# Kernel tuning notes

Hardware: AMD Instinct MI355X
Metric: run time of the kernel (lower is better)

Reference implementation:

```python
import jax, jax.numpy as jnp
import numpy as np

B, IN_DIM, N, L = 8, 2, 512, 64
D_MODEL = 32
D_FF = 32          # must equal D_MODEL: output_bn is BatchNorm2d(d_model) applied to skip
DEPTH = 3          # blocks=3 * layers=1; dilation resets to 1 each block -> all dilations = 1
KS = 2             # temporal kernel size
EPS = 1e-5         # BatchNorm eps


def setup_inputs() -> dict:
    key = jax.random.key(0)
    ks = jax.random.split(key, 16)
    s = 0.1  # weight scale for numeric sanity
    x = jax.random.normal(ks[0], (B, IN_DIM, N, L), jnp.float32)
    a = jax.random.uniform(ks[1], (N, N), jnp.float32)
    adj = a / a.sum(axis=1, keepdims=True)  # row-stochastic diffusion matrix
    return {
        "x": x,
        "adj": adj,
        "Wstart": jax.random.normal(ks[2], (D_MODEL, IN_DIM), jnp.float32) * s,
        "bstart": jnp.zeros((D_MODEL,), jnp.float32),
        "Wf": jax.random.normal(ks[3], (DEPTH, D_MODEL, D_MODEL, KS), jnp.float32) * s,
        "bf": jnp.zeros((DEPTH, D_MODEL), jnp.float32),
        "Wg": jax.random.normal(ks[4], (DEPTH, D_MODEL, D_MODEL, KS), jnp.float32) * s,
        "bg": jnp.zeros((DEPTH, D_MODEL), jnp.float32),
        "Wskip": jax.random.normal(ks[5], (DEPTH, D_FF, D_MODEL), jnp.float32) * s,
        "bskip": jnp.zeros((DEPTH, D_FF), jnp.float32),
        "Wgc": jax.random.normal(ks[6], (DEPTH, D_MODEL, 3 * D_MODEL), jnp.float32) * s,
        "bgc": jnp.zeros((DEPTH, D_MODEL), jnp.float32),
        "gcbn_g": jnp.ones((DEPTH, D_MODEL), jnp.float32),
        "gcbn_b": jnp.zeros((DEPTH, D_MODEL), jnp.float32),
        "bn_g": jnp.ones((DEPTH, D_MODEL), jnp.float32),
        "bn_b": jnp.zeros((DEPTH, D_MODEL), jnp.float32),
        "obn_g": jnp.ones((D_MODEL,), jnp.float32),
        "obn_b": jnp.zeros((D_MODEL,), jnp.float32),
    }


def _c1x1(x, W, b):
    # Conv2d with (1,1) kernel == channel mixing. x: [b,c,n,l], W: [o,c]
    return jnp.einsum('bcnl,oc->bonl', x, W) + b[None, :, None, None]


def _dconv(x, W, b, d):
    # Conv2d kernel (1,2), dilation d along time (valid). W: [o,c,2]
    Lx = x.shape[-1]
    y = (jnp.einsum('bcnl,oc->bonl', x[..., :Lx - d], W[..., 0])
         + jnp.einsum('bcnl,oc->bonl', x[..., d:], W[..., 1]))
    return y + b[None, :, None, None]


def _bn(x, g, bta):
    # eval-mode BatchNorm2d: running_mean=0, running_var=1
    inv = g / jnp.sqrt(1.0 + EPS)
    return x * inv[None, :, None, None] + bta[None, :, None, None]


def reference(x, adj, Wstart, bstart, Wf, bf, Wg, bg, Wskip, bskip,
              Wgc, bgc, gcbn_g, gcbn_b, bn_g, bn_b, obn_g, obn_b):
    rf = 1 + DEPTH * (KS - 1)  # receptive field with dilation 1 per layer
    h = _c1x1(x, Wstart, bstart)
    if h.shape[-1] < rf:
        h = jnp.pad(h, ((0, 0), (0, 0), (0, 0), (rf - h.shape[-1], 0)))
    skip = None
    for i in range(DEPTH):
        residual = h
        filt = jnp.tanh(_dconv(h, Wf[i], bf[i], 1))
        gate = jax.nn.sigmoid(_dconv(h, Wg[i], bg[i], 1))
        h = filt * gate
        s = _c1x1(h, Wskip[i], bskip[i])
        skip = s if skip is None else s + skip[..., -s.shape[-1]:]
        if i == DEPTH - 1:
            break
        # order-2 graph diffusion: h, A h, A^2 h -> concat -> 1x1 conv -> BN (dropout: eval noop)
        x1 = jnp.einsum('bcnl,nm->bcml', h, adj)
        x2 = jnp.einsum('bcnl,nm->bcml', x1, adj)
        cat = jnp.concatenate([h, x1, x2], axis=1)
        g = _bn(_c1x1(cat, Wgc[i], bgc[i]), gcbn_g[i], gcbn_b[i])
        h = g + residual[..., -g.shape[-1]:]
        h = _bn(h, bn_g[i], bn_b[i])
    out = _bn(skip, obn_g, obn_b)
    return jnp.swapaxes(out, 1, 3)  # [B, L', N, C]
```

## Files before the change

### kernel.cpp

```cpp
#include <hip/hip_runtime.h>
#include <hip/hip_bf16.h>

#define B_     8
#define CIN_   2
#define N_     512
#define C_     32
#define L_     64
#define LOUT_  61
#define BUF_   ((size_t)(8*32*512*64))

typedef __hip_bfloat16 bf16;
typedef unsigned short ushort_t;
typedef __attribute__((ext_vector_type(8))) unsigned short us8;
typedef __attribute__((ext_vector_type(8))) short bf16x8;
typedef __attribute__((ext_vector_type(4))) float f32x4;

static __device__ __forceinline__ float bits2f(ushort_t u) {
    return __uint_as_float(((unsigned)u) << 16);
}
static __device__ __forceinline__ ushort_t f2bits(float v) {
    unsigned u = __float_as_uint(v);
    return (ushort_t)((u + 0x7fffu + ((u >> 16) & 1u)) >> 16);
}

__global__ void k_start(const float* __restrict__ x,
                        const float* __restrict__ Wst,
                        const float* __restrict__ bst,
                        ushort_t* __restrict__ h) {
    int idx = blockIdx.x * 256 + threadIdx.x;
    int l0 = (idx & 7) * 8;
    int n  = (idx >> 3) & 511;
    int o  = (idx >> 12) & 31;
    int b  = idx >> 17;
    float w0 = Wst[o * 2], w1 = Wst[o * 2 + 1], bb = bst[o];
    int xbase = (b * CIN_ * N_ + n) * L_ + l0;
    float va[8], vb[8];
    *(float4*)&va[0] = *(const float4*)(x + xbase);
    *(float4*)&va[4] = *(const float4*)(x + xbase + 4);
    *(float4*)&vb[0] = *(const float4*)(x + xbase + N_ * L_);
    *(float4*)&vb[4] = *(const float4*)(x + xbase + N_ * L_ + 4);
    us8 r;
    #pragma unroll
    for (int k = 0; k < 8; ++k) r[k] = f2bits(bb + va[k] * w0 + vb[k] * w1);
    *(us8*)(h + (size_t)idx * 8) = r;
}

__global__ void k_transA(const float* __restrict__ adj, ushort_t* __restrict__ adjT) {
    __shared__ float buf[64][65];
    int ti = blockIdx.x & 7;
    int tj = blockIdx.x >> 3;
    int t = threadIdx.x;
    for (int r = 0; r < 16; ++r) {
        int e = t + 256 * r;
        int rl = e >> 6, cl = e & 63;
        buf[rl][cl] = adj[(size_t)(ti * 64 + rl) * 512 + tj * 64 + cl];
    }
    __syncthreads();
    for (int r = 0; r < 16; ++r) {
        int e = t + 256 * r;
        int ml = e >> 6, nl = e & 63;
        adjT[(size_t)(tj * 64 + ml) * 512 + ti * 64 + nl] = f2bits(buf[nl][ml]);
    }
}

__global__ __launch_bounds__(256, 2) void k_sq(const ushort_t* __restrict__ adjT,
                                               ushort_t* __restrict__ adj2T) {
    __shared__ __align__(16) ushort_t lds2[8192];
    ushort_t* As = lds2;
    ushort_t* Bs = lds2 + 4096;
    int mt = blockIdx.x & 7, nc = blockIdx.x >> 3;
    int t = threadIdx.x, lane = t & 63, w = t >> 6;
    int la = lane & 15, q = lane >> 4;
    f32x4 acc[4];
    #pragma unroll
    for (int mi = 0; mi < 4; ++mi) acc[mi] = (f32x4)0.f;
    for (int p0 = 0; p0 < 512; p0 += 64) {
        __syncthreads();
        #pragma unroll
        for (int r = 0; r < 2; ++r) {
            int e = t + 256 * r, ml = e >> 3, oct = e & 7;
            int sw = ((oct + (ml >> 3)) & 7) << 3;
            *(us8*)(As + ml * 64 + sw) =
                *(const us8*)(adjT + (size_t)(mt * 64 + ml) * 512 + p0 + oct * 8);
            *(us8*)(Bs + ml * 64 + sw) =
                *(const us8*)(adjT + (size_t)(p0 + ml) * 512 + nc * 64 + oct * 8);
        }
        __syncthreads();
        #pragma unroll
        for (int ks = 0; ks < 2; ++ks) {
            bf16x8 a[4];
            #pragma unroll
            for (int mi = 0; mi < 4; ++mi) {
                int m = mi * 16 + la;
                int bl = (ks * 4 + q + (m >> 3)) & 7;
                a[mi] = *(const bf16x8*)(As + m * 64 + bl * 8);
            }
            bf16x8 bv;
            {
                int n = w * 16 + la;
                int rot = ((n >> 3) + ks * 4 + q) & 7;
                int col = rot * 8 + (n & 7);
                const ushort_t* p = Bs + (ks * 32 + q * 8) * 64 + col;
                #pragma unroll
                for (int j = 0; j < 8; ++j) bv[j] = (short)p[j * 64];
            }
            #pragma unroll
            for (int mi = 0; mi < 4; ++mi)
                acc[mi] = __builtin_amdgcn_mfma_f32_16x16x32_bf16(a[mi], bv, acc[mi], 0, 0, 0);
        }
    }
    __syncthreads();
    ushort_t* Ys = lds2;
    #pragma unroll
    for (int mi = 0; mi < 4; ++mi)
        #pragma unroll
        for (int r = 0; r < 4; ++r)
            Ys[(mi * 16 + q * 4 + r) * 72 + w * 16 + la] = f2bits(acc[mi][r]);
    __syncthreads();
    #pragma unroll
    for (int r = 0; r < 2; ++r) {
        int e = t + 256 * r, ml = e >> 3, oct = e & 7;
        us8 v = *(const us8*)(Ys + ml * 72 + oct * 8);
        *(us8*)(adj2T + (size_t)(mt * 64 + ml) * 512 + nc * 64 + oct * 8) = v;
    }
}

__global__ __launch_bounds__(256, 2) void k_gs_mfma(
        const ushort_t* __restrict__ h,
        const float* __restrict__ Wf, const float* __restrict__ bfp,
        const float* __restrict__ Wg, const float* __restrict__ bgp,
        const float* __restrict__ Wsk, const float* __restrict__ bsk,
        ushort_t* __restrict__ G, float* __restrict__ out,
        int off, int mode, int storeG,
        const float* __restrict__ og, const float* __restrict__ obb) {
    __shared__ __align__(16) ushort_t Hs[128 * 72];
    __shared__ __align__(16) ushort_t Asf[32 * 72];
    __shared__ __align__(16) ushort_t Asg[32 * 72];
    __shared__ __align__(16) ushort_t As2[32 * 40];
    __shared__ float bfv[32], bgv[32], bsv[32];
    int t = threadIdx.x;
    int b = blockIdx.x >> 7, n0 = (blockIdx.x & 127) * 4;
    int lane = t & 63, w = t >> 6;
    int la = lane & 15, q = lane >> 4;

    {
        int o = t >> 3, k8 = (t & 7) * 8;
        us8 vf, vg;
        #pragma unroll
        for (int i = 0; i < 8; ++i) {
            int k = k8 + i, c = k & 31, tap = k >> 5;
            vf[i] = f2bits(Wf[o * 64 + c * 2 + tap]);
            vg[i] = f2bits(Wg[o * 64 + c * 2 + tap]);
        }
        *(us8*)(Asf + o * 72 + k8) = vf;
        *(us8*)(Asg + o * 72 + k8) = vg;
        if (k8 < 32) {
            us8 vs;
            #pragma unroll
            for (int i = 0; i < 8; ++i) vs[i] = f2bits(Wsk[o * 32 + k8 + i]);
            *(us8*)(As2 + o * 40 + k8) = vs;
        }
        if (t < 32) { bfv[t] = bfp[t]; bgv[t] = bgp[t]; bsv[t] = bsk[t]; }
    }
    const ushort_t* hb = h + (size_t)(b * 32) * 512 * 64;
    #pragma unroll
    for (int r = 0; r < 4; ++r) {
        int e = t + 256 * r;
        int row = e >> 3, oct = e & 7;
        us8 v = *(const us8*)(hb + ((size_t)(row >> 2) * 512 + n0 + (row & 3)) * 64 + oct * 8);
        int sw = (oct + row + (row >> 5)) & 7;
        *(us8*)(Hs + row * 72 + sw * 8) = v;
    }
    {
        int row = t >> 1, hf = t & 1;
        *(uint2*)(Hs + row * 72 + 64 + hf * 4) = make_uint2(0u, 0u);
    }
    __syncthreads();

    bf16x8 af[2][2], ag[2][2];
    #pragma unroll
    for (int mt = 0; mt < 2; ++mt)
        #pragma unroll
        for (int ks = 0; ks < 2; ++ks) {
            af[mt][ks] = *(const bf16x8*)(Asf + (mt * 16 + la) * 72 + ks * 32 + q * 8);
            ag[mt][ks] = *(const bf16x8*)(Asg + (mt * 16 + la) * 72 + ks * 32 + q * 8);
        }

    f32x4 fa[2][4], ga[2][4];
    #pragma unroll
    for (int mt = 0; mt < 2; ++mt)
        #pragma unroll
        for (int ct = 0; ct < 4; ++ct) { fa[mt][ct] = (f32x4)0.f; ga[mt][ct] = (f32x4)0.f; }
    #pragma unroll
    for (int ct = 0; ct < 4; ++ct) {
        #pragma unroll
        for (int ks = 0; ks < 2; ++ks) {
            int le = ct * 16 + la + ks;
            bf16x8 bv;
            #pragma unroll
            for (int j = 0; j < 8; ++j) {
                int row = 32 * q + 4 * j + w;
                int pos = (le < 64) ? ((((le >> 3) + row + q) & 7) * 8 + (le & 7)) : le;
                bv[j] = (short)Hs[row * 72 + pos];
            }
            #pragma unroll
            for (int mt = 0; mt < 2; ++mt) {
                fa[mt][ct] = __builtin_amdgcn_mfma_f32_16x16x32_bf16(af[mt][ks], bv, fa[mt][ct], 0, 0, 0);
                ga[mt][ct] = __builtin_amdgcn_mfma_f32_16x16x32_bf16(ag[mt][ks], bv, ga[mt][ct], 0, 0, 0);
            }
        }
    }

    #pragma unroll
    for (int mt = 0; mt < 2; ++mt)
        #pragma unroll
        for (int ct = 0; ct < 4; ++ct)
            #pragma unroll
            for (int r = 0; r < 4; ++r) {
                int o = mt * 16 + q * 4 + r;
                float fv = fa[mt][ct][r] + bfv[o];
                float gv = ga[mt][ct][r] + bgv[o];
                float ef = __expf(2.f * fv);
                float act = (1.f - 2.f / (ef + 1.f)) * (1.f / (1.f + __expf(-gv)));
                int l = ct * 16 + la;
                int row = o * 4 + w;
                int sw = ((l >> 3) + row + (row >> 5)) & 7;
                Hs[row * 72 + sw * 8 + (l & 7)] = f2bits(act);
            }

    bf16x8 a2[2];
    a2[0] = *(const bf16x8*)(As2 + la * 40 + q * 8);
    a2[1] = *(const bf16x8*)(As2 + (16 + la) * 40 + q * 8);
    f32x4 sa[2][4];
    #pragma unroll
    for (int mt = 0; mt < 2; ++mt)
        #pragma unroll
        for (int ct = 0; ct < 4; ++ct) sa[mt][ct] = (f32x4)0.f;
    #pragma unroll
    for (int ct = 0; ct < 4; ++ct) {
        int le = ct * 16 + la + off;
        bf16x8 bv;
        #pragma unroll
        for (int j = 0; j < 8; ++j) {
            int row = 32 * q + 4 * j + w;
            int pos = (le < 64) ? ((((le >> 3) + row + q) & 7) * 8 + (le & 7)) : le;
            bv[j] = (short)Hs[row * 72 + pos];
        }
        sa[0][ct] = __builtin_amdgcn_mfma_f32_16x16x32_bf16(a2[0], bv, sa[0][ct], 0, 0, 0);
        sa[1][ct] = __builtin_amdgcn_mfma_f32_16x16x32_bf16(a2[1], bv, sa[1][ct], 0, 0, 0);
    }
    __syncthreads();

    if (storeG) {
        #pragma unroll
        for (int r = 0; r < 4; ++r) {
            int e = t + 256 * r;
            int row = e >> 3, oct = e & 7;
            int sw = (oct + row + (row >> 5)) & 7;
            us8 v = *(const us8*)(Hs + row * 72 + sw * 8);
            *(us8*)(G + ((size_t)(b * 32 + (row >> 2)) * 512 + n0 + (row & 3)) * 64 + oct * 8) = v;
        }
    }
    __syncthreads();

    float* St = (float*)Hs;
    const float rbn = rsqrtf(1.f + 1e-5f);
    #pragma unroll
    for (int half = 0; half < 2; ++half) {
        if ((w >> 1) == half) {
            #pragma unroll
            for (int mt = 0; mt < 2; ++mt)
                #pragma unroll
                for (int ct = 0; ct < 4; ++ct) {
                    int col = (w & 1) * 64 + ct * 16 + la;
                    int ob = mt * 16 + q * 4;
                    float4 sv = make_float4(sa[mt][ct][0] + bsv[ob],
                                            sa[mt][ct][1] + bsv[ob + 1],
                                            sa[mt][ct][2] + bsv[ob + 2],
                                            sa[mt][ct][3] + bsv[ob + 3]);
                    *(float4*)(St + col * 36 + ob) = sv;
                }
        }
        __syncthreads();
        {
            int col = t >> 1, o0 = (t & 1) * 16;
            int nr = half * 2 + (col >> 6), l = col & 63;
            if (l < LOUT_) {
                float* po = out + ((size_t)(b * LOUT_ + l) * 512 + n0 + nr) * 32 + o0;
                #pragma unroll
                for (int i = 0; i < 4; ++i) {
                    float4 s = *(float4*)(St + col * 36 + o0 + i * 4);
                    if (mode == 0) {
                        *(float4*)(po + i * 4) = s;
                    } else {
                        float4 old = *(float4*)(po + i * 4);
                        float4 vv = make_float4(old.x + s.x, old.y + s.y,
                                                old.z + s.z, old.w + s.w);
                        if (mode == 2) {
                            int ob = o0 + i * 4;
                            vv.x = vv.x * (og[ob] * rbn) + obb[ob];
                            vv.y = vv.y * (og[ob + 1] * rbn) + obb[ob + 1];
                            vv.z = vv.z * (og[ob + 2] * rbn) + obb[ob + 2];
                            vv.w = vv.w * (og[ob + 3] * rbn) + obb[ob + 3];
                        }
                        *(float4*)(po + i * 4) = vv;
                    }
                }
            }
        }
        __syncthreads();
    }
}

__global__ __launch_bounds__(256, 2) void k_diffuse2(
        const ushort_t* __restrict__ X, const ushort_t* __restrict__ adjT,
        const ushort_t* __restrict__ adj2T,
        ushort_t* __restrict__ Y1, ushort_t* __restrict__ Y2) {
    __shared__ __align__(16) ushort_t lds[16384];
    ushort_t* As1 = lds;
    ushort_t* As2 = lds + 4096;
    ushort_t* Xs  = lds + 8192;
    int cp = blockIdx.x & 15;
    int mt = (blockIdx.x >> 4) & 7;
    int b  = blockIdx.x >> 7;
    int t  = threadIdx.x;
    int lane = t & 63, w = t >> 6;
    int c_loc = w & 1, lh = w >> 1;
    int m0 = mt * 64;
    int la = lane & 15, q = lane >> 4;
    const ushort_t* Xb = X + (size_t)(b * 32 + cp * 2) * 512 * 64;
    f32x4 acc1[4][2], acc2[4][2];
    #pragma unroll
    for (int mi = 0; mi < 4; ++mi)
        #pragma unroll
        for (int li = 0; li < 2; ++li) { acc1[mi][li] = (f32x4)0.f; acc2[mi][li] = (f32x4)0.f; }

    for (int n0 = 0; n0 < 512; n0 += 64) {
        __syncthreads();
        #pragma unroll
        for (int r = 0; r < 2; ++r) {
            int e = t + 256 * r;
            int ml = e >> 3, oct = e & 7;
            int sw = ((oct + (ml >> 3)) & 7) << 3;
            *(us8*)(As1 + ml * 64 + sw) =
                *(const us8*)(adjT + (size_t)(m0 + ml) * 512 + n0 + oct * 8);
            *(us8*)(As2 + ml * 64 + sw) =
                *(const us8*)(adj2T + (size_t)(m0 + ml) * 512 + n0 + oct * 8);
        }
        #pragma unroll
        for (int r = 0; r < 4; ++r) {
            int e = t + 256 * r;
            int cl = e >> 9, nl = (e >> 3) & 63, oct = e & 7;
            us8 v = *(const us8*)(Xb + ((size_t)cl * 512 + n0 + nl) * 64 + oct * 8);
            *(us8*)(Xs + cl * 4096 + nl * 64 + (((oct + (nl >> 3)) & 7) << 3)) = v;
        }
        __syncthreads();
        #pragma unroll
        for (int ks = 0; ks < 2; ++ks) {
            bf16x8 a1[4], a2v[4];
            #pragma unroll
            for (int mi = 0; mi < 4; ++mi) {
                int m = mi * 16 + la;
                int bl = (ks * 4 + q + (m >> 3)) & 7;
                a1[mi]  = *(const bf16x8*)(As1 + m * 64 + bl * 8);
                a2v[mi] = *(const bf16x8*)(As2 + m * 64 + bl * 8);
            }
            bf16x8 bb[2];
            #pragma unroll
            for (int li = 0; li < 2; ++li) {
                int l = lh * 32 + li * 16 + la;
                int rot = ((l >> 3) + ks * 4 + q) & 7;
                int col = rot * 8 + (l & 7);
                const ushort_t* p = Xs + c_loc * 4096 + (ks * 32 + q * 8) * 64 + col;
                bf16x8 v;
                #pragma unroll
                for (int j = 0; j < 8; ++j) v[j] = (short)p[j * 64];
                bb[li] = v;
            }
            #pragma unroll
            for (int mi = 0; mi < 4; ++mi)
                #pragma unroll
                for (int li = 0; li < 2; ++li) {
                    acc1[mi][li] = __builtin_amdgcn_mfma_f32_16x16x32_bf16(a1[mi], bb[li], acc1[mi][li], 0, 0, 0);
                    acc2[mi][li] = __builtin_amdgcn_mfma_f32_16x16x32_bf16(a2v[mi], bb[li], acc2[mi][li], 0, 0, 0);
                }
        }
    }
    ushort_t* Ys = lds;
    #pragma unroll
    for (int pass = 0; pass < 2; ++pass) {
        __syncthreads();
        f32x4 (*src)[2] = pass ? acc2 : acc1;
        #pragma unroll
        for (int mi = 0; mi < 4; ++mi)
            #pragma unroll
            for (int li = 0; li < 2; ++li)
                #pragma unroll
                for (int r = 0; r < 4; ++r) {
                    int row = mi * 16 + q * 4 + r;
                    int col = lh * 32 + li * 16 + la;
                    Ys[c_loc * 4608 + row * 72 + col] = f2bits(src[mi][li][r]);
                }
        __syncthreads();
        ushort_t* Yo = pass ? Y2 : Y1;
        int c = t >> 7, mrem = t & 127;
        int m = mrem >> 1, lq = mrem & 1;
        #pragma unroll
        for (int r = 0; r < 4; ++r) {
            int l0 = lq * 32 + r * 8;
            us8 v = *(const us8*)(Ys + c * 4608 + m * 72 + l0);
            *(us8*)(Yo + ((size_t)(b * 32 + cp * 2 + c) * 512 + m0 + m) * 64 + l0) = v;
        }
    }
}

__global__ __launch_bounds__(256, 2) void k_gc3_mfma(
        ushort_t* __restrict__ G, const ushort_t* __restrict__ X1,
        const ushort_t* __restrict__ X2, const ushort_t* __restrict__ hres,
        const float* __restrict__ Wgc, const float* __restrict__ bgc,
        const float* __restrict__ gg, const float* __restrict__ gb,
        const float* __restrict__ bg2, const float* __restrict__ bb2) {
    __shared__ __align__(16) ushort_t cat[384 * 72];
    __shared__ __align__(16) ushort_t hr[128 * 64];
    __shared__ __align__(16) ushort_t Aw[32 * 104];
    __shared__ float prm[5][32];
    int t = threadIdx.x;
    int b = blockIdx.x >> 7, n0 = (blockIdx.x & 127) * 4;
    int lane = t & 63, w = t >> 6;
    int la = lane & 15, q = lane >> 4;

    #pragma unroll
    for (int r = 0; r < 12; ++r) {
        int e = t + 256 * r;
        int row = e >> 3, oct = e & 7;
        int k = row >> 2;
        const ushort_t* src = (k < 32) ? G : ((k < 64) ? X1 : X2);
        us8 v = *(const us8*)(src + ((size_t)(b * 32 + (k & 31)) * 512 + n0 + (row & 3)) * 64 + oct * 8);
        int sw = (oct + row + (row >> 5)) & 7;
        *(us8*)(cat + row * 72 + sw * 8) = v;
    }
    #pragma unroll
    for (int r = 0; r < 4; ++r) {
        int e = t + 256 * r;
        int row = e >> 3, oct = e & 7;
        us8 v = *(const us8*)(hres + ((size_t)(b * 32 + (row >> 2)) * 512 + n0 + (row & 3)) * 64 + oct * 8);
        *(us8*)(hr + row * 64 + oct * 8) = v;
    }
    for (int e = t; e < 384; e += 256) {
        int o = e / 12, oct = e % 12;
        us8 v;
        #pragma unroll
        for (int i = 0; i < 8; ++i) v[i] = f2bits(Wgc[o * 96 + oct * 8 + i]);
        *(us8*)(Aw + o * 104 + oct * 8) = v;
    }
    if (t < 32) {
        prm[0][t] = bgc[t]; prm[1][t] = gg[t]; prm[2][t] = gb[t];
        prm[3][t] = bg2[t]; prm[4][t] = bb2[t];
    }
    __syncthreads();

    bf16x8 a[2][3];
    #pragma unroll
    for (int mt = 0; mt < 2; ++mt)
        #pragma unroll
        for (int ks = 0; ks < 3; ++ks)
            a[mt][ks] = *(const bf16x8*)(Aw + (mt * 16 + la) * 104 + ks * 32 + q * 8);

    f32x4 acc[2][4];
    #pragma unroll
    for (int mt = 0; mt < 2; ++mt)
        #pragma unroll
        for (int ct = 0; ct < 4; ++ct) acc[mt][ct] = (f32x4)0.f;
    #pragma unroll
    for (int ct = 0; ct < 4; ++ct) {
        int le = ct * 16 + la;
        #pragma unroll
        for (int ks = 0; ks < 3; ++ks) {
            bf16x8 bv;
            #pragma unroll
            for (int j = 0; j < 8; ++j) {
                int row = (ks * 32 + q * 8 + j) * 4 + w;
                int sw = ((le >> 3) + row + (row >> 5)) & 7;
                bv[j] = (short)cat[row * 72 + sw * 8 + (le & 7)];
            }
            acc[0][ct] = __builtin_amdgcn_mfma_f32_16x16x32_bf16(a[0][ks], bv, acc[0][ct], 0, 0, 0);
            acc[1][ct] = __builtin_amdgcn_mfma_f32_16x16x32_bf16(a[1][ks], bv, acc[1][ct], 0, 0, 0);
        }
    }
    __syncthreads();

    const float rbn = rsqrtf(1.f + 1e-5f);
    #pragma unroll
    for (int mt = 0; mt < 2; ++mt)
        #pragma unroll
        for (int ct = 0; ct < 4; ++ct)
            #pragma unroll
            for (int r = 0; r < 4; ++r) {
                int o = mt * 16 + q * 4 + r;
                int l = ct * 16 + la;
                float v = acc[mt][ct][r] + prm[0][o];
                v = v * (prm[1][o] * rbn) + prm[2][o];
                float res = (l < 63) ? bits2f(hr[(o * 4 + w) * 64 + l + 1]) : 0.f;
                v = (v + res) * (prm[3][o] * rbn) + prm[4][o];
                int row = o * 4 + w;
                int sw = ((l >> 3) + row + (row >> 5)) & 7;
                cat[row * 72 + sw * 8 + (l & 7)] = f2bits(v);
            }
    __syncthreads();
    #pragma unroll
    for (int r = 0; r < 4; ++r) {
        int e = t + 256 * r;
        int row = e >> 3, oct = e & 7;
        int sw = (oct + row + (row >> 5)) & 7;
        us8 v = *(const us8*)(cat + row * 72 + sw * 8);
        *(us8*)(G + ((size_t)(b * 32 + (row >> 2)) * 512 + n0 + (row & 3)) * 64 + oct * 8) = v;
    }
}

extern "C" void kernel_launch(void* const* d_in, const int* in_sizes, int n_in,
                              void* d_out, int out_size, void* d_ws, size_t ws_size,
                              hipStream_t stream) {
    const float* x      = (const float*)d_in[0];
    const float* adj    = (const float*)d_in[1];
    const float* Wstart = (const float*)d_in[2];
    const float* bstart = (const float*)d_in[3];
    const float* Wf     = (const float*)d_in[4];
    const float* bf_    = (const float*)d_in[5];
    const float* Wg     = (const float*)d_in[6];
    const float* bg     = (const float*)d_in[7];
    const float* Wskip  = (const float*)d_in[8];
    const float* bskip  = (const float*)d_in[9];
    const float* Wgc    = (const float*)d_in[10];
    const float* bgc    = (const float*)d_in[11];
    const float* gcbn_g = (const float*)d_in[12];
    const float* gcbn_b = (const float*)d_in[13];
    const float* bn_g   = (const float*)d_in[14];
    const float* bn_b   = (const float*)d_in[15];
    const float* obn_g  = (const float*)d_in[16];
    const float* obn_b  = (const float*)d_in[17];
    float* out = (float*)d_out;

    ushort_t* P0    = (ushort_t*)d_ws;
    ushort_t* P1    = P0 + BUF_;
    ushort_t* P2    = P1 + BUF_;
    ushort_t* P3    = P2 + BUF_;
    ushort_t* adjT  = P3 + BUF_;
    ushort_t* adj2T = adjT + 512 * 512;

    k_transA<<<64, 256, 0, stream>>>(adj, adjT);
    k_sq<<<64, 256, 0, stream>>>(adjT, adj2T);
    k_start<<<4096, 256, 0, stream>>>(x, Wstart, bstart, P0);

    ushort_t* h  = P0;
    ushort_t* Gb = P1;
    for (int i = 0; i < 3; ++i) {
        int mode = (i == 0) ? 0 : ((i == 2) ? 2 : 1);
        k_gs_mfma<<<1024, 256, 0, stream>>>(h, Wf + i * 2048, bf_ + i * 32,
                                            Wg + i * 2048, bg + i * 32,
                                            Wskip + i * 1024, bskip + i * 32,
                                            Gb, out, 2 - i, mode, (i < 2) ? 1 : 0,
                                            obn_g, obn_b);
        if (i == 2) break;
        k_diffuse2<<<1024, 256, 0, stream>>>(Gb, adjT, adj2T, P2, P3);
        k_gc3_mfma<<<1024, 256, 0, stream>>>(Gb, P2, P3, h,
                                             Wgc + i * 3072, bgc + i * 32,
                                             gcbn_g + i * 32, gcbn_b + i * 32,
                                             bn_g + i * 32, bn_b + i * 32);
        ushort_t* tmp = h; h = Gb; Gb = tmp;
    }
}
```

Baseline: 317.8 us.

## Stage h channel-innermost in LDS and transpose G before diffusion

The gated-conv kernel now stages its input tile in LDS as [node][time][channel], so each MFMA B operand is one vector load instead of eight scattered scalar LDS reads. A new transpose kernel rewrites G into a [c][l][n] layout, and a new diffusion kernel reads that layout with contiguous node-major loads. The transpose only runs when the workspace is large enough, otherwise the old diffusion kernel is kept. This trades an extra launch and a full read and write of G per layer for cheaper operand staging in the diffusion GEMM.

Result: slower. 336.2 us (+5.8%).

```diff
diff --git a/kernel.cpp b/kernel.cpp
--- a/kernel.cpp
+++ b/kernel.cpp
@@ -125,14 +125,41 @@
     }
 }
 
+__global__ void k_transG(const ushort_t* __restrict__ Gsrc, ushort_t* __restrict__ GT) {
+    __shared__ __align__(16) ushort_t buf[64 * 72];
+    int b  = blockIdx.x >> 8;
+    int c  = (blockIdx.x >> 3) & 31;
+    int nt = blockIdx.x & 7;
+    int t = threadIdx.x;
+    size_t base = (size_t)(b * 32 + c) * 32768;
+    int n0 = nt * 64;
+    #pragma unroll
+    for (int r = 0; r < 2; ++r) {
+        int e = t + 256 * r;
+        int n = e & 63, loct = e >> 6;
+        us8 v = *(const us8*)(Gsrc + base + (size_t)(n0 + n) * 64 + loct * 8);
+        #pragma unroll
+        for (int k = 0; k < 8; ++k) buf[(loct * 8 + k) * 72 + n] = v[k];
+    }
+    __syncthreads();
+    #pragma unroll
+    for (int r = 0; r < 2; ++r) {
+        int e = t + 256 * r;
+        int oct = e & 7, l = (e >> 3) & 63;
+        us8 v = *(const us8*)(buf + l * 72 + oct * 8);
+        *(us8*)(GT + base + (size_t)l * 512 + n0 + oct * 8) = v;
+    }
+}
+
 __global__ __launch_bounds__(256, 2) void k_gs_mfma(
         const ushort_t* __restrict__ h,
         const float* __restrict__ Wf, const float* __restrict__ bfp,
         const float* __restrict__ Wg, const float* __restrict__ bgp,
         const float* __restrict__ Wsk, const float* __restrict__ bsk,
         ushort_t* __restrict__ G, float* __restrict__ out,
-        int off, int mode, int storeG,
+        int Llen, int off, int mode, int storeG,
         const float* __restrict__ og, const float* __restrict__ obb) {
+    __shared__ __align__(16) ushort_t Ht[4 * 66 * 40];
     __shared__ __align__(16) ushort_t Hs[128 * 72];
     __shared__ __align__(16) ushort_t Asf[32 * 72];
     __shared__ __align__(16) ushort_t Asg[32 * 72];
@@ -162,18 +189,25 @@
         }
         if (t < 32) { bfv[t] = bfp[t]; bgv[t] = bgp[t]; bsv[t] = bsk[t]; }
     }
+    #pragma unroll
+    for (int r = 0; r < 2; ++r) {
+        int idx = t + 256 * r;
+        int lz = Llen + (idx >> 7);
+        int node = (idx >> 5) & 3, c = idx & 31;
+        if (lz < 66) Ht[(node * 66 + lz) * 40 + c] = 0;
+    }
     const ushort_t* hb = h + (size_t)(b * 32) * 512 * 64;
     #pragma unroll
     for (int r = 0; r < 4; ++r) {
         int e = t + 256 * r;
-        int row = e >> 3, oct = e & 7;
-        us8 v = *(const us8*)(hb + ((size_t)(row >> 2) * 512 + n0 + (row & 3)) * 64 + oct * 8);
-        int sw = (oct + row + (row >> 5)) & 7;
-        *(us8*)(Hs + row * 72 + sw * 8) = v;
-    }
-    {
-        int row = t >> 1, hf = t & 1;
-        *(uint2*)(Hs + row * 72 + 64 + hf * 4) = make_uint2(0u, 0u);
+        int row = e & 127, loct = e >> 7;
+        int c = row >> 2, node = row & 3;
+        us8 v = *(const us8*)(hb + ((size_t)c * 512 + n0 + node) * 64 + loct * 8);
+        #pragma unroll
+        for (int k = 0; k < 8; ++k) {
+            int l = loct * 8 + k;
+            if (l < Llen) Ht[(node * 66 + l) * 40 + c] = v[k];
+        }
     }
     __syncthreads();
 
@@ -193,16 +227,10 @@
         for (int ct = 0; ct < 4; ++ct) { fa[mt][ct] = (f32x4)0.f; ga[mt][ct] = (f32x4)0.f; }
     #pragma unroll
     for (int ct = 0; ct < 4; ++ct) {
+        int lcol = ct * 16 + la;
         #pragma unroll
         for (int ks = 0; ks < 2; ++ks) {
-            int le = ct * 16 + la + ks;
-            bf16x8 bv;
-            #pragma unroll
-            for (int j = 0; j < 8; ++j) {
-                int row = 32 * q + 4 * j + w;
-                int pos = (le < 64) ? ((((le >> 3) + row + q) & 7) * 8 + (le & 7)) : le;
-                bv[j] = (short)Hs[row * 72 + pos];
-            }
+            bf16x8 bv = *(const bf16x8*)(Ht + (w * 66 + lcol + ks) * 40 + q * 8);
             #pragma unroll
             for (int mt = 0; mt < 2; ++mt) {
                 fa[mt][ct] = __builtin_amdgcn_mfma_f32_16x16x32_bf16(af[mt][ks], bv, fa[mt][ct], 0, 0, 0);
@@ -312,7 +340,105 @@
     }
 }
 
-__global__ __launch_bounds__(256, 2) void k_diffuse2(
+__global__ __launch_bounds__(256, 2) void k_diffuse2_gt(
+        const ushort_t* __restrict__ GT, const ushort_t* __restrict__ adjT,
+        const ushort_t* __restrict__ adj2T,
+        ushort_t* __restrict__ Y1, ushort_t* __restrict__ Y2) {
+    __shared__ __align__(16) ushort_t lds[16384];
+    ushort_t* As1 = lds;
+    ushort_t* As2 = lds + 4096;
+    ushort_t* Xs  = lds + 8192;
+    int cp = blockIdx.x & 15;
+    int mt = (blockIdx.x >> 4) & 7;
+    int b  = blockIdx.x >> 7;
+    int t  = threadIdx.x;
+    int lane = t & 63, w = t >> 6;
+    int c_loc = w & 1, lh = w >> 1;
+    int m0 = mt * 64;
+    int la = lane & 15, q = lane >> 4;
+    const ushort_t* GTb = GT + (size_t)(b * 32 + cp * 2) * 32768;
+    f32x4 acc1[4][2], acc2[4][2];
+    #pragma unroll
+    for (int mi = 0; mi < 4; ++mi)
+        #pragma unroll
+        for (int li = 0; li < 2; ++li) { acc1[mi][li] = (f32x4)0.f; acc2[mi][li] = (f32x4)0.f; }
+
+    for (int n0 = 0; n0 < 512; n0 += 64) {
+        __syncthreads();
+        #pragma unroll
+        for (int r = 0; r < 2; ++r) {
+            int e = t + 256 * r;
+            int ml = e >> 3, oct = e & 7;
+            int sw = ((oct + (ml >> 3)) & 7) << 3;
+            *(us8*)(As1 + ml * 64 + sw) =
+                *(const us8*)(adjT + (size_t)(m0 + ml) * 512 + n0 + oct * 8);
+            *(us8*)(As2 + ml * 64 + sw) =
+                *(const us8*)(adj2T + (size_t)(m0 + ml) * 512 + n0 + oct * 8);
+        }
+        #pragma unroll
+        for (int r = 0; r < 4; ++r) {
+            int e = t + 256 * r;
+            int row = e >> 3, oct = e & 7;
+            int cl = row >> 6, l = row & 63;
+            us8 v = *(const us8*)(GTb + (size_t)cl * 32768 + (size_t)l * 512 + n0 + oct * 8);
+            *(us8*)(Xs + cl * 4096 + l * 64 + (((oct + (l >> 3)) & 7) << 3)) = v;
+        }
+        __syncthreads();
+        #pragma unroll
+        for (int ks = 0; ks < 2; ++ks) {
+            bf16x8 a1[4], a2v[4];
+            #pragma unroll
+            for (int mi = 0; mi < 4; ++mi) {
+                int m = mi * 16 + la;
+                int bl = (ks * 4 + q + (m >> 3)) & 7;
+                a1[mi]  = *(const bf16x8*)(As1 + m * 64 + bl * 8);
+                a2v[mi] = *(const bf16x8*)(As2 + m * 64 + bl * 8);
+            }
+            bf16x8 bb[2];
+            #pragma unroll
+            for (int li = 0; li < 2; ++li) {
+                int l = lh * 32 + li * 16 + la;
+                int bl = (ks * 4 + q + (l >> 3)) & 7;
+                bb[li] = *(const bf16x8*)(Xs + c_loc * 4096 + l * 64 + bl * 8);
+            }
+            #pragma unroll
+            for (int mi = 0; mi < 4; ++mi)
+                #pragma unroll
+                for (int li = 0; li < 2; ++li) {
+                    acc1[mi][li] = __builtin_amdgcn_mfma_f32_16x16x32_bf16(a1[mi], bb[li], acc1[mi][li], 0, 0, 0);
+                    acc2[mi][li] = __builtin_amdgcn_mfma_f32_16x16x32_bf16(a2v[mi], bb[li], acc2[mi][li], 0, 0, 0);
+                }
+        }
+    }
+    ushort_t* Ys = lds;
+    #pragma unroll
+    for (int pass = 0; pass < 2; ++pass) {
+        __syncthreads();
+        f32x4 (*src)[2] = pass ? acc2 : acc1;
+        #pragma unroll
+        for (int mi = 0; mi < 4; ++mi)
+            #pragma unroll
+            for (int li = 0; li < 2; ++li)
+                #pragma unroll
+                for (int r = 0; r < 4; ++r) {
+                    int row = mi * 16 + q * 4 + r;
+                    int col = lh * 32 + li * 16 + la;
+                    Ys[c_loc * 4608 + row * 72 + col] = f2bits(src[mi][li][r]);
+                }
+        __syncthreads();
+        ushort_t* Yo = pass ? Y2 : Y1;
+        int c = t >> 7, mrem = t & 127;
+        int m = mrem >> 1, lq = mrem & 1;
+        #pragma unroll
+        for (int r = 0; r < 4; ++r) {
+            int l0 = lq * 32 + r * 8;
+            us8 v = *(const us8*)(Ys + c * 4608 + m * 72 + l0);
+            *(us8*)(Yo + ((size_t)(b * 32 + cp * 2 + c) * 512 + m0 + m) * 64 + l0) = v;
+        }
+    }
+}
+
+__global__ __launch_bounds__(256, 2) void k_diffuse2_cnl(
         const ushort_t* __restrict__ X, const ushort_t* __restrict__ adjT,
         const ushort_t* __restrict__ adj2T,
         ushort_t* __restrict__ Y1, ushort_t* __restrict__ Y2) {
@@ -334,7 +460,6 @@
     for (int mi = 0; mi < 4; ++mi)
         #pragma unroll
         for (int li = 0; li < 2; ++li) { acc1[mi][li] = (f32x4)0.f; acc2[mi][li] = (f32x4)0.f; }
-
     for (int n0 = 0; n0 < 512; n0 += 64) {
         __syncthreads();
         #pragma unroll
@@ -546,6 +671,8 @@
     ushort_t* P3    = P2 + BUF_;
     ushort_t* adjT  = P3 + BUF_;
     ushort_t* adj2T = adjT + 512 * 512;
+    ushort_t* GT    = adj2T + 512 * 512;
+    bool use_gt = ws_size >= 2ull * (5 * BUF_ + 2 * 512 * 512);
 
     k_transA<<<64, 256, 0, stream>>>(adj, adjT);
     k_sq<<<64, 256, 0, stream>>>(adjT, adj2T);
@@ -558,10 +685,15 @@
         k_gs_mfma<<<1024, 256, 0, stream>>>(h, Wf + i * 2048, bf_ + i * 32,
                                             Wg + i * 2048, bg + i * 32,
                                             Wskip + i * 1024, bskip + i * 32,
-                                            Gb, out, 2 - i, mode, (i < 2) ? 1 : 0,
+                                            Gb, out, L_ - i, 2 - i, mode, (i < 2) ? 1 : 0,
                                             obn_g, obn_b);
         if (i == 2) break;
-        k_diffuse2<<<1024, 256, 0, stream>>>(Gb, adjT, adj2T, P2, P3);
+        if (use_gt) {
+            k_transG<<<2048, 256, 0, stream>>>(Gb, GT);
+            k_diffuse2_gt<<<1024, 256, 0, stream>>>(GT, adjT, adj2T, P2, P3);
+        } else {
+            k_diffuse2_cnl<<<1024, 256, 0, stream>>>(Gb, adjT, adj2T, P2, P3);
+        }
         k_gc3_mfma<<<1024, 256, 0, stream>>>(Gb, P2, P3, h,
                                              Wgc + i * 3072, bgc + i * 32,
                                              gcbn_g + i * 32, gcbn_b + i * 32,
```

## Pre-transpose G so diffusion B-operand loads become vectorized LDS reads

Applied to the files above, without the earlier changes.

Adds a transpose kernel that writes G in [b,c,l,n] layout, so the diffusion kernel can stage it with a row-wise swizzle and load MFMA B fragments as single 16-byte LDS reads instead of eight strided scalar reads. The gated-conv kernel now stages h into a channel-minor LDS tile (Ht) so its B operand is also one vector load, and it zero-pads the time positions past Llen. The swizzle pattern changes in k_sq and the diffusion kernel, and launch bounds rise to 3 waves. The cost is an extra kernel launch and an extra global read and write of G for each diffusion layer, plus scattered scalar LDS writes during staging.

Measured after the change: 334.3 us. 5.2% more time.

```diff
diff --git a/kernel.cpp b/kernel.cpp
--- a/kernel.cpp
+++ b/kernel.cpp
@@ -79,7 +79,7 @@
         #pragma unroll
         for (int r = 0; r < 2; ++r) {
             int e = t + 256 * r, ml = e >> 3, oct = e & 7;
-            int sw = ((oct + (ml >> 3)) & 7) << 3;
+            int sw = ((oct + ml) & 7) << 3;
             *(us8*)(As + ml * 64 + sw) =
                 *(const us8*)(adjT + (size_t)(mt * 64 + ml) * 512 + p0 + oct * 8);
             *(us8*)(Bs + ml * 64 + sw) =
@@ -92,17 +92,26 @@
             #pragma unroll
             for (int mi = 0; mi < 4; ++mi) {
                 int m = mi * 16 + la;
-                int bl = (ks * 4 + q + (m >> 3)) & 7;
+                int bl = (ks * 4 + q + m) & 7;
                 a[mi] = *(const bf16x8*)(As + m * 64 + bl * 8);
             }
             bf16x8 bv;
             {
                 int n = w * 16 + la;
-                int rot = ((n >> 3) + ks * 4 + q) & 7;
+                int rot = (n + ks * 4 + q) & 7;
                 int col = rot * 8 + (n & 7);
-                const ushort_t* p = Bs + (ks * 32 + q * 8) * 64 + col;
+                const ushort_t* p = Bs + (ks * 32 + q * 8) * 64;
+                bf16x8 v;
                 #pragma unroll
-                for (int j = 0; j < 8; ++j) bv[j] = (short)p[j * 64];
+                for (int j = 0; j < 8; ++j) {
+                    int row = ks * 32 + q * 8 + j;
+                    int bl2 = (q + ks * 4 + row) & 7;
+                    (void)bl2;
+                    int blk = ((n >> 3) + row) & 7;
+                    v[j] = (short)Bs[row * 64 + blk * 8 + (n & 7)];
+                }
+                (void)p; (void)rot; (void)col;
+                bv = v;
             }
             #pragma unroll
             for (int mi = 0; mi < 4; ++mi)
@@ -122,6 +131,32 @@
         int e = t + 256 * r, ml = e >> 3, oct = e & 7;
         us8 v = *(const us8*)(Ys + ml * 72 + oct * 8);
         *(us8*)(adj2T + (size_t)(mt * 64 + ml) * 512 + nc * 64 + oct * 8) = v;
+    }
+}
+
+__global__ void k_transG(const ushort_t* __restrict__ Gsrc, ushort_t* __restrict__ GT) {
+    __shared__ __align__(16) ushort_t buf[64 * 72];
+    int b  = blockIdx.x >> 8;
+    int c  = (blockIdx.x >> 3) & 31;
+    int nt = blockIdx.x & 7;
+    int t = threadIdx.x;
+    size_t base = (size_t)(b * 32 + c) * 32768;
+    int n0 = nt * 64;
+    #pragma unroll
+    for (int r = 0; r < 2; ++r) {
+        int e = t + 256 * r;
+        int n = e & 63, loct = e >> 6;
+        us8 v = *(const us8*)(Gsrc + base + (size_t)(n0 + n) * 64 + loct * 8);
+        #pragma unroll
+        for (int k = 0; k < 8; ++k) buf[(loct * 8 + k) * 72 + n] = v[k];
+    }
+    __syncthreads();
+    #pragma unroll
+    for (int r = 0; r < 2; ++r) {
+        int e = t + 256 * r;
+        int oct = e & 7, l = (e >> 3) & 63;
+        us8 v = *(const us8*)(buf + l * 72 + oct * 8);
+        *(us8*)(GT + base + (size_t)l * 512 + n0 + oct * 8) = v;
     }
 }
 
@@ -131,8 +166,9 @@
         const float* __restrict__ Wg, const float* __restrict__ bgp,
         const float* __restrict__ Wsk, const float* __restrict__ bsk,
         ushort_t* __restrict__ G, float* __restrict__ out,
-        int off, int mode, int storeG,
+        int Llen, int off, int mode, int storeG,
         const float* __restrict__ og, const float* __restrict__ obb) {
+    __shared__ __align__(16) ushort_t Ht[4 * 66 * 40];
     __shared__ __align__(16) ushort_t Hs[128 * 72];
     __shared__ __align__(16) ushort_t Asf[32 * 72];
     __shared__ __align__(16) ushort_t Asg[32 * 72];
@@ -162,18 +198,25 @@
         }
         if (t < 32) { bfv[t] = bfp[t]; bgv[t] = bgp[t]; bsv[t] = bsk[t]; }
     }
+    #pragma unroll
+    for (int r = 0; r < 2; ++r) {
+        int idx = t + 256 * r;
+        int lz = Llen + (idx >> 7);
+        int node = (idx >> 5) & 3, c = idx & 31;
+        if (lz < 66) Ht[(node * 66 + lz) * 40 + c] = 0;
+    }
     const ushort_t* hb = h + (size_t)(b * 32) * 512 * 64;
     #pragma unroll
     for (int r = 0; r < 4; ++r) {
         int e = t + 256 * r;
-        int row = e >> 3, oct = e & 7;
-        us8 v = *(const us8*)(hb + ((size_t)(row >> 2) * 512 + n0 + (row & 3)) * 64 + oct * 8);
-        int sw = (oct + row + (row >> 5)) & 7;
-        *(us8*)(Hs + row * 72 + sw * 8) = v;
-    }
-    {
-        int row = t >> 1, hf = t & 1;
-        *(uint2*)(Hs + row * 72 + 64 + hf * 4) = make_uint2(0u, 0u);
+        int row = e & 127, loct = e >> 7;
+        int c = row >> 2, node = row & 3;
+        us8 v = *(const us8*)(hb + ((size_t)c * 512 + n0 + node) * 64 + loct * 8);
+        #pragma unroll
+        for (int k = 0; k < 8; ++k) {
+            int l = loct * 8 + k;
+            if (l < Llen) Ht[(node * 66 + l) * 40 + c] = v[k];
+        }
     }
     __syncthreads();
 
@@ -193,16 +236,10 @@
         for (int ct = 0; ct < 4; ++ct) { fa[mt][ct] = (f32x4)0.f; ga[mt][ct] = (f32x4)0.f; }
     #pragma unroll
     for (int ct = 0; ct < 4; ++ct) {
+        int lcol = ct * 16 + la;
         #pragma unroll
         for (int ks = 0; ks < 2; ++ks) {
-            int le = ct * 16 + la + ks;
-            bf16x8 bv;
-            #pragma unroll
-            for (int j = 0; j < 8; ++j) {
-                int row = 32 * q + 4 * j + w;
-                int pos = (le < 64) ? ((((le >> 3) + row + q) & 7) * 8 + (le & 7)) : le;
-                bv[j] = (short)Hs[row * 72 + pos];
-            }
+            bf16x8 bv = *(const bf16x8*)(Ht + (w * 66 + lcol + ks) * 40 + q * 8);
             #pragma unroll
             for (int mt = 0; mt < 2; ++mt) {
                 fa[mt][ct] = __builtin_amdgcn_mfma_f32_16x16x32_bf16(af[mt][ks], bv, fa[mt][ct], 0, 0, 0);
@@ -312,8 +349,8 @@
     }
 }
 
-__global__ __launch_bounds__(256, 2) void k_diffuse2(
-        const ushort_t* __restrict__ X, const ushort_t* __restrict__ adjT,
+__global__ __launch_bounds__(256, 3) void k_diffuse2_gt(
+        const ushort_t* __restrict__ GT, const ushort_t* __restrict__ adjT,
         const ushort_t* __restrict__ adj2T,
         ushort_t* __restrict__ Y1, ushort_t* __restrict__ Y2) {
     __shared__ __align__(16) ushort_t lds[16384];
@@ -328,7 +365,7 @@
     int c_loc = w & 1, lh = w >> 1;
     int m0 = mt * 64;
     int la = lane & 15, q = lane >> 4;
-    const ushort_t* Xb = X + (size_t)(b * 32 + cp * 2) * 512 * 64;
+    const ushort_t* GTb = GT + (size_t)(b * 32 + cp * 2) * 32768;
     f32x4 acc1[4][2], acc2[4][2];
     #pragma unroll
     for (int mi = 0; mi < 4; ++mi)
@@ -341,7 +378,7 @@
         for (int r = 0; r < 2; ++r) {
             int e = t + 256 * r;
             int ml = e >> 3, oct = e & 7;
-            int sw = ((oct + (ml >> 3)) & 7) << 3;
+            int sw = ((oct + ml) & 7) << 3;
             *(us8*)(As1 + ml * 64 + sw) =
                 *(const us8*)(adjT + (size_t)(m0 + ml) * 512 + n0 + oct * 8);
             *(us8*)(As2 + ml * 64 + sw) =
@@ -350,9 +387,10 @@
         #pragma unroll
         for (int r = 0; r < 4; ++r) {
             int e = t + 256 * r;
-            int cl = e >> 9, nl = (e >> 3) & 63, oct = e & 7;
-            us8 v = *(const us8*)(Xb + ((size_t)cl * 512 + n0 + nl) * 64 + oct * 8);
-            *(us8*)(Xs + cl * 4096 + nl * 64 + (((oct + (nl >> 3)) & 7) << 3)) = v;
+            int row = e >> 3, oct = e & 7;
+            int cl = row >> 6, l = row & 63;
+            us8 v = *(const us8*)(GTb + (size_t)cl * 32768 + (size_t)l * 512 + n0 + oct * 8);
+            *(us8*)(Xs + cl * 4096 + l * 64 + (((oct + l) & 7) << 3)) = v;
         }
         __syncthreads();
         #pragma unroll
@@ -361,7 +399,7 @@
             #pragma unroll
             for (int mi = 0; mi < 4; ++mi) {
                 int m = mi * 16 + la;
-                int bl = (ks * 4 + q + (m >> 3)) & 7;
+                int bl = (ks * 4 + q + m) & 7;
                 a1[mi]  = *(const bf16x8*)(As1 + m * 64 + bl * 8);
                 a2v[mi] = *(const bf16x8*)(As2 + m * 64 + bl * 8);
             }
@@ -369,13 +407,8 @@
             #pragma unroll
             for (int li = 0; li < 2; ++li) {
                 int l = lh * 32 + li * 16 + la;
-                int rot = ((l >> 3) + ks * 4 + q) & 7;
-                int col = rot * 8 + (l & 7);
-                const ushort_t* p = Xs + c_loc * 4096 + (ks * 32 + q * 8) * 64 + col;
-                bf16x8 v;
-                #pragma unroll
-                for (int j = 0; j < 8; ++j) v[j] = (short)p[j * 64];
-                bb[li] = v;
+                int bl = (ks * 4 + q + l) & 7;
+                bb[li] = *(const bf16x8*)(Xs + c_loc * 4096 + l * 64 + bl * 8);
             }
             #pragma unroll
             for (int mi = 0; mi < 4; ++mi)
@@ -546,6 +579,7 @@
     ushort_t* P3    = P2 + BUF_;
     ushort_t* adjT  = P3 + BUF_;
     ushort_t* adj2T = adjT + 512 * 512;
+    ushort_t* GT    = adj2T + 512 * 512;
 
     k_transA<<<64, 256, 0, stream>>>(adj, adjT);
     k_sq<<<64, 256, 0, stream>>>(adjT, adj2T);
@@ -558,10 +592,11 @@
         k_gs_mfma<<<1024, 256, 0, stream>>>(h, Wf + i * 2048, bf_ + i * 32,
                                             Wg + i * 2048, bg + i * 32,
                                             Wskip + i * 1024, bskip + i * 32,
-                                            Gb, out, 2 - i, mode, (i < 2) ? 1 : 0,
+                                            Gb, out, L_ - i, 2 - i, mode, (i < 2) ? 1 : 0,
                                             obn_g, obn_b);
         if (i == 2) break;
-        k_diffuse2<<<1024, 256, 0, stream>>>(Gb, adjT, adj2T, P2, P3);
+        k_transG<<<2048, 256, 0, stream>>>(Gb, GT);
+        k_diffuse2_gt<<<1024, 256, 0, stream>>>(GT, adjT, adj2T, P2, P3);
         k_gc3_mfma<<<1024, 256, 0, stream>>>(Gb, P2, P3, h,
                                              Wgc + i * 3072, bgc + i * 32,
                                              gcbn_g + i * 32, gcbn_b + i * 32,
```
